# Kernel tuning notes

Hardware: AMD Instinct MI355X
Metric: run time of the kernel (lower is better)

Reference implementation:

```python
import jax, jax.numpy as jnp
import numpy as np
from jax import lax

EPS = 1e-8

def setup_inputs() -> dict:
    key = jax.random.key(0)
    ks = jax.random.split(key, 9)
    B, Cin, H, W = 16, 128, 64, 64
    C = 256
    return {
        "x":  jax.random.normal(ks[0], (B, Cin, H, W), jnp.float32),
        "w1": jax.random.normal(ks[1], (C, Cin, 3, 3), jnp.float32) * 0.02,
        "b1": jax.random.normal(ks[2], (C,), jnp.float32) * 0.02,
        "w2": jax.random.normal(ks[3], (C, C), jnp.float32) * 0.02,
        "b2": jax.random.normal(ks[4], (C,), jnp.float32) * 0.02,
        "w3": jax.random.normal(ks[5], (C, C), jnp.float32) * 0.02,
        "b3": jax.random.normal(ks[6], (C,), jnp.float32) * 0.02,
        "w4": jax.random.normal(ks[7], (C, C), jnp.float32) * 0.02,
        "b4": jax.random.normal(ks[8], (C,), jnp.float32) * 0.02,
    }

def reference(x, w1, b1, w2, b2, w3, b3, w4, b4):
    B = x.shape[0]
    # conv1: 3x3, pad 1 -> [B, 256, H, W]
    conv1 = lax.conv_general_dilated(
        x, w1, window_strides=(1, 1), padding="SAME",
        dimension_numbers=("NCHW", "OIHW", "NCHW")) + b1[None, :, None, None]
    H, W = conv1.shape[2], conv1.shape[3]
    C = conv1.shape[1]
    # gap1 -> [B, 256]; note: forward never applies relu/sigmoid (faithful)
    gap1 = conv1.mean(axis=(2, 3))
    c2 = gap1 @ w2.T + b2            # 1x1 conv on 1x1 spatial == dense
    c3 = c2 @ w3.T + b3              # [B, 256]
    # add1 = conv1 + conv1 * c3 (broadcast scale over spatial)
    add1 = conv1 * (1.0 + c3[:, :, None, None])
    gap2 = add1.mean(axis=(2, 3))    # [B, 256]
    # cosine similarity along channel dim between gap2 and add1 -> [B, H, W]
    num = jnp.einsum("bc,bchw->bhw", gap2, add1)
    n_g = jnp.maximum(jnp.linalg.norm(gap2, axis=1), EPS)[:, None, None]
    n_a = jnp.maximum(jnp.sqrt(jnp.sum(add1 * add1, axis=1)), EPS)
    cos = num / (n_g * n_a)
    r1 = cos.reshape(B, H * W)       # [B, HW]
    m1 = r1.T @ r1                   # [HW, HW] cross-batch position similarity
    # conv4: 1x1 conv -> [B, 256, H, W]
    conv4 = jnp.einsum("oc,bchw->bohw", w4, add1) + b4[None, :, None, None]
    # torch: permute to NHWC then view as [B, 256, HW] (mixes dims; faithful)
    r2 = jnp.transpose(conv4, (0, 2, 3, 1)).reshape(B, C, H * W)
    m2 = r2 @ m1                     # [B, 256, HW]
    return m2.reshape(B, C, H, W)
```

## Files before the change

### kernel.cpp

```cpp
#include <hip/hip_runtime.h>

#define EPSF 1e-8f

typedef __attribute__((ext_vector_type(8))) short bf16x8;
typedef __attribute__((ext_vector_type(16))) float f32x16;

#define MFMA32(a, b, c) __builtin_amdgcn_mfma_f32_32x32x16_bf16(a, b, c, 0, 0, 0)

__device__ __forceinline__ uint32_t splitpack(float v) {
    uint32_t u = __float_as_uint(v);
    uint32_t hb = (u + 0x7fffu + ((u >> 16) & 1u)) & 0xffff0000u;
    float rem = v - __uint_as_float(hb);
    uint32_t r = __float_as_uint(rem);
    uint32_t lb = (r + 0x7fffu + ((r >> 16) & 1u)) >> 16;
    return (hb >> 16) | (lb << 16);
}
__device__ __forceinline__ float unpackf(uint32_t p) {
    return __uint_as_float(p << 16) + __uint_as_float(p & 0xffff0000u);
}

__device__ __forceinline__ void gload_lds16(const void* src, void* dst) {
#if __has_builtin(__builtin_amdgcn_global_load_lds)
    __builtin_amdgcn_global_load_lds(
        (const __attribute__((address_space(1))) uint32_t*)src,
        (__attribute__((address_space(3))) uint32_t*)dst, 16, 0, 0);
#else
    *(uint4*)dst = *(const uint4*)src;
#endif
}

__global__ __launch_bounds__(256) void k_xpack(const float* __restrict__ x,
                                               unsigned short* __restrict__ xph,
                                               unsigned short* __restrict__ xpl) {
    const int bx = blockIdx.x;
    const int hb = bx & 15, cg = (bx >> 4) & 15, b = bx >> 8;
    const int tid = threadIdx.x;
    const int w = tid & 63, hs = tid >> 6;
    const int h = hb * 4 + hs;
    uint32_t hiw[4], low[4];
#pragma unroll
    for (int q = 0; q < 4; ++q) {
        uint32_t u0 = splitpack(x[(((b * 128 + cg * 8 + q * 2) * 64) + h) * 64 + w]);
        uint32_t u1 = splitpack(x[(((b * 128 + cg * 8 + q * 2 + 1) * 64) + h) * 64 + w]);
        hiw[q] = (u0 & 0xffffu) | (u1 << 16);
        low[q] = (u0 >> 16) | (u1 & 0xffff0000u);
    }
    const long o = ((((long)(b * 16 + cg) * 64 + h) * 64) + w) * 8;
    *(uint4*)(xph + o) = *(uint4*)hiw;
    *(uint4*)(xpl + o) = *(uint4*)low;
}

__global__ __launch_bounds__(256) void k_wpack(const float* __restrict__ w1,
                                               short* __restrict__ Bh, short* __restrict__ Bl) {
    int d = blockIdx.x * 256 + threadIdx.x;
    int j = d & 7, lane = (d >> 3) & 63, nt = (d >> 9) & 7, cp = (d >> 12) & 7, tap = d >> 15;
    int oc = nt * 32 + (lane & 31);
    int cin = cp * 16 + (lane >> 5) * 8 + j;
    uint32_t u = splitpack(w1[oc * 1152 + cin * 9 + tap]);
    Bh[d] = (short)(u & 0xffffu);
    Bl[d] = (short)(u >> 16);
}

__global__ __launch_bounds__(512, 4) void k_conv1(
        const unsigned short* __restrict__ xph, const unsigned short* __restrict__ xpl,
        const short* __restrict__ Bh, const short* __restrict__ Bl,
        const float* __restrict__ b1,
        uint32_t* __restrict__ c1p, float* __restrict__ gpart) {
    __shared__ uint4 lds[2 * 2 * 12 * 66];
    const int bx = blockIdx.x;
    const int ot = bx & 1, hp = (bx >> 1) & 15, b = bx >> 5;
    const int h0 = hp * 4;
    const int tid = threadIdx.x;
    const int lane = tid & 63, wv = tid >> 6;
    const int mq = wv >> 1, nh = wv & 1;
    const int l31 = lane & 31, hbit = lane >> 5;

    f32x16 acc[2][2];
#pragma unroll
    for (int i = 0; i < 2; ++i)
#pragma unroll
        for (int j = 0; j < 2; ++j)
#pragma unroll
            for (int r = 0; r < 16; ++r) acc[i][j][r] = 0.f;

    auto stage = [&](int buf, int cp) {
#pragma unroll
        for (int i = 0; i < 3; ++i) {
            const int id = wv * 3 + i;
            const int plane = (id >= 12) ? 1 : 0;
            const int u = id - plane * 12;
            const int r6 = u >> 1, kg = u & 1;
            const int grow = h0 - 1 + r6;
            uint4* dst = &lds[((buf * 2 + plane) * 12 + u) * 66 + 1 + lane];
            if ((unsigned)grow < 64u) {
                const unsigned short* pls = plane ? xpl : xph;
                const unsigned short* src =
                    pls + ((((long)(b * 16 + cp * 2 + kg) * 64 + grow) * 64) + lane) * 8;
                gload_lds16(src, dst);
            } else {
                *dst = (uint4){0u, 0u, 0u, 0u};
            }
        }
    };

    stage(0, 0);
    if (tid < 96) {
        const int row = tid >> 1, side = tid & 1;
        lds[row * 66 + (side ? 65 : 0)] = (uint4){0u, 0u, 0u, 0u};
    }
    __syncthreads();

    int buf = 0;
    for (int cp = 0; cp < 8; ++cp) {
        if (cp < 7) stage(buf ^ 1, cp + 1);
        bf16x8 Bhv[2][2], Blv[2][2];
#define LOADB(tap, par) do {                                                      \
            _Pragma("unroll")                                                     \
            for (int nt = 0; nt < 2; ++nt) {                                      \
                const int fi = (((tap) * 8 + cp) * 8 + ot * 4 + nh * 2 + nt) * 512 + lane * 8; \
                Bhv[par][nt] = *(const bf16x8*)(Bh + fi);                         \
                Blv[par][nt] = *(const bf16x8*)(Bl + fi);                         \
            } } while (0)
        LOADB(0, 0);
#pragma unroll
        for (int tap = 0; tap < 9; ++tap) {
            const int cur = tap & 1, nxt = cur ^ 1;
            if (tap < 8) LOADB(tap + 1, nxt);
            const int kh = tap / 3, kw = tap % 3;
            bf16x8 ah[2], al[2];
#pragma unroll
            for (int mt = 0; mt < 2; ++mt) {
                const int rb = ((buf * 2 + 0) * 12 + (mq + kh) * 2 + hbit) * 66
                               + kw + mt * 32 + l31;
                ah[mt] = *(const bf16x8*)&lds[rb];
                al[mt] = *(const bf16x8*)&lds[rb + 12 * 66];
            }
            __builtin_amdgcn_s_setprio(1);
#pragma unroll
            for (int nt = 0; nt < 2; ++nt)
#pragma unroll
                for (int mt = 0; mt < 2; ++mt) {
                    acc[mt][nt] = MFMA32(ah[mt], Bhv[cur][nt], acc[mt][nt]);
                    acc[mt][nt] = MFMA32(ah[mt], Blv[cur][nt], acc[mt][nt]);
                    acc[mt][nt] = MFMA32(al[mt], Bhv[cur][nt], acc[mt][nt]);
                }
            __builtin_amdgcn_s_setprio(0);
        }
#undef LOADB
        __syncthreads();
        buf ^= 1;
    }

    const int hrow = h0 + mq;
#pragma unroll
    for (int nt = 0; nt < 2; ++nt) {
        const int oc = ot * 128 + (nh * 2 + nt) * 32 + l31;
        float g = 0.f;
#pragma unroll
        for (int mt = 0; mt < 2; ++mt)
#pragma unroll
            for (int r = 0; r < 16; ++r) g += acc[mt][nt][r];
        g += __shfl_xor(g, 32);
        if (hbit == 0) gpart[((b * 16 + hp) * 4 + mq) * 256 + oc] = g;
        const float bias = b1[oc];
#pragma unroll
        for (int mt = 0; mt < 2; ++mt) {
#pragma unroll
            for (int r = 0; r < 16; ++r) {
                const int row = (r & 3) + 8 * (r >> 2) + 4 * hbit;
                const int p = hrow * 64 + mt * 32 + row;
                c1p[((long)(b * 4096 + p)) * 256 + oc] = splitpack(acc[mt][nt][r] + bias);
            }
        }
    }
}

__global__ __launch_bounds__(256) void k_mlp(const float* __restrict__ gpart,
                                             const float* __restrict__ b1,
                                             const float* __restrict__ w2, const float* __restrict__ b2,
                                             const float* __restrict__ w3, const float* __restrict__ b3,
                                             float* __restrict__ scale, float* __restrict__ ga,
                                             float* __restrict__ n_g) {
    int b = blockIdx.x, tid = threadIdx.x;
    __shared__ float gs[256], c2s[256], red[4];
    float g = 0.f;
#pragma unroll 8
    for (int i = 0; i < 64; ++i) g += gpart[(b * 64 + i) * 256 + tid];
    gs[tid] = g * (1.f / 4096.f) + b1[tid];
    __syncthreads();
    {
        const float4* wr = (const float4*)(w2 + tid * 256);
        float a = b2[tid];
#pragma unroll 8
        for (int c4 = 0; c4 < 64; c4++) {
            float4 wv = wr[c4];
            a += wv.x * gs[c4*4] + wv.y * gs[c4*4+1] + wv.z * gs[c4*4+2] + wv.w * gs[c4*4+3];
        }
        c2s[tid] = a;
    }
    __syncthreads();
    float a3 = b3[tid];
    {
        const float4* wr = (const float4*)(w3 + tid * 256);
#pragma unroll 8
        for (int c4 = 0; c4 < 64; c4++) {
            float4 wv = wr[c4];
            a3 += wv.x * c2s[c4*4] + wv.y * c2s[c4*4+1] + wv.z * c2s[c4*4+2] + wv.w * c2s[c4*4+3];
        }
    }
    float s1 = 1.f + a3;
    float g2 = gs[tid] * s1;
    scale[b * 256 + tid] = s1;
    ga[b * 256 + tid] = g2 * s1;
    float r = g2 * g2;
    for (int off = 32; off; off >>= 1) r += __shfl_down(r, off);
    if ((tid & 63) == 0) red[tid >> 6] = r;
    __syncthreads();
    if (tid == 0) n_g[b] = fmaxf(sqrtf(red[0] + red[1] + red[2] + red[3]), EPSF);
}

__global__ __launch_bounds__(256) void k_cos(
        const uint32_t* __restrict__ c1p,
        const float* __restrict__ scale, const float* __restrict__ ga,
        const float* __restrict__ n_g, float* __restrict__ r1) {
    const int bx = blockIdx.x;
    const int pt = bx & 63, b = bx >> 6;
    const int tid = threadIdx.x;
    const int lane = tid & 63, wv = tid >> 6;
    const int half = lane >> 5, l31 = lane & 31;
    float ga8[8], sc8[8];
#pragma unroll
    for (int q = 0; q < 8; ++q) {
        ga8[q] = ga[b * 256 + l31 * 8 + q];
        sc8[q] = scale[b * 256 + l31 * 8 + q];
    }
    const float ng = n_g[b];
#pragma unroll
    for (int pp = 0; pp < 8; ++pp) {
        const int p = pt * 64 + wv * 16 + pp * 2 + half;
        const uint32_t* base = c1p + ((long)(b * 4096 + p)) * 256 + l31 * 8;
        uint4 a = *(const uint4*)base;
        uint4 bq = *(const uint4*)(base + 4);
        uint32_t pk[8] = {a.x, a.y, a.z, a.w, bq.x, bq.y, bq.z, bq.w};
        float num = 0.f, den = 0.f;
#pragma unroll
        for (int q = 0; q < 8; ++q) {
            const float v = unpackf(pk[q]);
            num += ga8[q] * v;
            const float t = sc8[q] * v;
            den += t * t;
        }
#pragma unroll
        for (int off = 1; off <= 16; off <<= 1) {
            num += __shfl_xor(num, off);
            den += __shfl_xor(den, off);
        }
        if (l31 == 0) {
            float na = fmaxf(sqrtf(den), EPSF);
            r1[b * 4096 + p] = num / (ng * na);
        }
    }
}

__global__ __launch_bounds__(256) void k_u(const float* __restrict__ r1,
                                           const float* __restrict__ w4,
                                           const float* __restrict__ b4,
                                           float* __restrict__ Uf, float* __restrict__ Dpart) {
    const int g = blockIdx.x;
    const int tid = threadIdx.x;
    __shared__ float rs[256], red[4];
    rs[tid] = r1[(g >> 4) * 4096 + (g & 15) * 256 + tid];
    __syncthreads();
    float a = 0.f;
#pragma unroll 8
    for (int o = 0; o < 256; ++o) a += rs[o] * w4[o * 256 + tid];
    Uf[(g >> 4) * 4096 + (g & 15) * 256 + tid] = a;
    float d = b4[tid] * rs[tid];
    for (int off = 32; off; off >>= 1) d += __shfl_down(d, off);
    if ((tid & 63) == 0) red[tid >> 6] = d;
    __syncthreads();
    if (tid == 0) Dpart[g] = red[0] + red[1] + red[2] + red[3];
}

__global__ __launch_bounds__(256) void k_t2(const uint32_t* __restrict__ c1p,
                                            const float* __restrict__ Uf,
                                            const float* __restrict__ scale,
                                            const float* __restrict__ Dpart,
                                            float* __restrict__ tmat) {
    __shared__ float Ac[16][256];
    __shared__ float Bc[16][260];
    __shared__ float scs[256];
    const int bx = blockIdx.x;
    const int b = bx >> 4, it = bx & 15;
    const int tid = threadIdx.x;
    const int il = tid >> 4, bp = tid & 15;
    scs[tid] = scale[b * 256 + tid];
    float acc = 0.f;
    for (int jc = 0; jc < 16; ++jc) {
        __syncthreads();
#pragma unroll
        for (int q = 0; q < 4; ++q) {
            const int f4i = tid + q * 256;
            const int row = f4i >> 6, col4 = f4i & 63;
            uint4 u = *(const uint4*)(c1p +
                ((long)(b * 4096 + it * 256 + row * 16 + jc)) * 256 + col4 * 4);
            Ac[row][col4 * 4 + 0] = unpackf(u.x) * scs[col4 * 4 + 0];
            Ac[row][col4 * 4 + 1] = unpackf(u.y) * scs[col4 * 4 + 1];
            Ac[row][col4 * 4 + 2] = unpackf(u.z) * scs[col4 * 4 + 2];
            Ac[row][col4 * 4 + 3] = unpackf(u.w) * scs[col4 * 4 + 3];
            *(float4*)&Bc[row][col4 * 4] =
                *(const float4*)(Uf + (long)row * 4096 + jc * 256 + col4 * 4);
        }
        __syncthreads();
#pragma unroll 8
        for (int j = 0; j < 256; j += 4) {
            float4 a4  = *(const float4*)&Ac[il][j];
            float4 b4v = *(const float4*)&Bc[bp][j];
            acc += a4.x * b4v.x + a4.y * b4v.y + a4.z * b4v.z + a4.w * b4v.w;
        }
    }
    float D = 0.f;
#pragma unroll
    for (int pr = 0; pr < 16; ++pr) D += Dpart[bp * 16 + pr];
    tmat[((b * 256) + it * 16 + il) * 16 + bp] = acc + D;
}

__global__ __launch_bounds__(256) void k_m2(const float* __restrict__ tmat,
                                            const float* __restrict__ r1,
                                            float* __restrict__ outb) {
    __shared__ float r1s[16][512];
    __shared__ float ts[256];
    int bx = blockIdx.x;
    int b = bx >> 7, it = (bx >> 3) & 15, pc = bx & 7;
    int tid = threadIdx.x;
    ts[tid] = tmat[(b * 256 + it * 16) * 16 + tid];
#pragma unroll
    for (int k = 0; k < 8; k++) {
        int f4i = tid + k * 256;
        int row = f4i >> 7, col = f4i & 127;
        *(float4*)&r1s[row][col * 4] = *(const float4*)(r1 + ((long)row << 12) + pc * 512 + col * 4);
    }
    __syncthreads();
    for (int il = 0; il < 16; il++) {
        float tv[16];
#pragma unroll
        for (int bp = 0; bp < 16; bp++) tv[bp] = ts[il * 16 + bp];
#pragma unroll
        for (int k = 0; k < 2; k++) {
            int p = k * 256 + tid;
            float s = 0.f;
#pragma unroll
            for (int bp = 0; bp < 16; bp++) s += tv[bp] * r1s[bp][p];
            outb[((long)b << 20) + ((long)(it * 16 + il) << 12) + pc * 512 + p] = s;
        }
    }
}

extern "C" void kernel_launch(void* const* d_in, const int* in_sizes, int n_in,
                              void* d_out, int out_size, void* d_ws, size_t ws_size,
                              hipStream_t stream) {
    const float* x  = (const float*)d_in[0];
    const float* w1 = (const float*)d_in[1];
    const float* b1 = (const float*)d_in[2];
    const float* w2 = (const float*)d_in[3];
    const float* b2 = (const float*)d_in[4];
    const float* w3 = (const float*)d_in[5];
    const float* b3 = (const float*)d_in[6];
    const float* w4 = (const float*)d_in[7];
    const float* b4 = (const float*)d_in[8];
    float* out = (float*)d_out;

    unsigned short* xph = (unsigned short*)d_out;
    unsigned short* xpl = xph + 8388608L;

    char* p = (char*)d_ws;
    uint32_t* c1p = (uint32_t*)p;  p += 16777216L * 4;
    short* Bh  = (short*)p;  p += 294912L * 2;
    short* Bl  = (short*)p;  p += 294912L * 2;
    float* gpart = (float*)p; p += 262144L * 4;
    float* scale = (float*)p; p += 4096L * 4;
    float* ga    = (float*)p; p += 4096L * 4;
    float* n_g   = (float*)p; p += 16L * 4;
    float* r1    = (float*)p; p += 65536L * 4;
    float* tmat  = (float*)p; p += 65536L * 4;
    float* Uf    = (float*)p; p += 65536L * 4;
    float* Dpart = (float*)p; p += 256L * 4;

    k_xpack <<<4096, 256, 0, stream>>>(x, xph, xpl);
    k_wpack <<<1152, 256, 0, stream>>>(w1, Bh, Bl);
    k_conv1 <<<512,  512, 0, stream>>>(xph, xpl, Bh, Bl, b1, c1p, gpart);
    k_mlp   <<<16,   256, 0, stream>>>(gpart, b1, w2, b2, w3, b3, scale, ga, n_g);
    k_cos   <<<1024, 256, 0, stream>>>(c1p, scale, ga, n_g, r1);
    k_u     <<<256,  256, 0, stream>>>(r1, w4, b4, Uf, Dpart);
    k_t2    <<<256,  256, 0, stream>>>(c1p, Uf, scale, Dpart, tmat);
    k_m2    <<<2048, 256, 0, stream>>>(tmat, r1, out);
}
```

Measured before the change: 252.7 us.

## Deepen conv1 operand prefetch pipeline and swizzle block order

The conv1 MFMA loop now prefetches weight fragments two taps ahead using a triple buffer that carries across channel-pair iterations. It also double-buffers the LDS A-fragment reads one tap ahead, so load latency overlaps with MFMA issue. Block indices are remapped so consecutive blocks land on different batch groups, which changes L2/XCD locality. Launch bounds are relaxed to one block per SM to free registers for the extra buffers, at the cost of lower occupancy.

```diff
diff --git a/kernel.cpp b/kernel.cpp
--- a/kernel.cpp
+++ b/kernel.cpp
@@ -61,13 +61,14 @@
     Bl[d] = (short)(u >> 16);
 }
 
-__global__ __launch_bounds__(512, 4) void k_conv1(
+__global__ __launch_bounds__(512, 1) void k_conv1(
         const unsigned short* __restrict__ xph, const unsigned short* __restrict__ xpl,
         const short* __restrict__ Bh, const short* __restrict__ Bl,
         const float* __restrict__ b1,
         uint32_t* __restrict__ c1p, float* __restrict__ gpart) {
     __shared__ uint4 lds[2 * 2 * 12 * 66];
-    const int bx = blockIdx.x;
+    const int bxr = blockIdx.x;
+    const int bx = ((bxr & 7) << 6) | (bxr >> 3);
     const int ot = bx & 1, hp = (bx >> 1) & 15, b = bx >> 5;
     const int h0 = hp * 4;
     const int tid = threadIdx.x;
@@ -110,46 +111,55 @@
     }
     __syncthreads();
 
+    bf16x8 Ahv[2][2], Alv[2][2], Bhv[3][2], Blv[3][2];
+#define LOADA(tap_, par) do {                                                     \
+        const int kh_ = (tap_) / 3, kw_ = (tap_) % 3;                             \
+        _Pragma("unroll")                                                         \
+        for (int mt = 0; mt < 2; ++mt) {                                          \
+            const int rb = ((buf * 2 + 0) * 12 + (mq + kh_) * 2 + hbit) * 66      \
+                           + kw_ + mt * 32 + l31;                                 \
+            Ahv[par][mt] = *(const bf16x8*)&lds[rb];                              \
+            Alv[par][mt] = *(const bf16x8*)&lds[rb + 12 * 66];                    \
+        } } while (0)
+#define LOADB(cp_, tap_, par) do {                                                \
+        _Pragma("unroll")                                                         \
+        for (int nt = 0; nt < 2; ++nt) {                                          \
+            const int fi = (((tap_) * 8 + (cp_)) * 8 + ot * 4 + nh * 2 + nt) * 512 + lane * 8; \
+            Bhv[par][nt] = *(const bf16x8*)(Bh + fi);                             \
+            Blv[par][nt] = *(const bf16x8*)(Bl + fi);                             \
+        } } while (0)
+
+    LOADB(0, 0, 0);
+    LOADB(0, 1, 1);
     int buf = 0;
     for (int cp = 0; cp < 8; ++cp) {
         if (cp < 7) stage(buf ^ 1, cp + 1);
-        bf16x8 Bhv[2][2], Blv[2][2];
-#define LOADB(tap, par) do {                                                      \
-            _Pragma("unroll")                                                     \
-            for (int nt = 0; nt < 2; ++nt) {                                      \
-                const int fi = (((tap) * 8 + cp) * 8 + ot * 4 + nh * 2 + nt) * 512 + lane * 8; \
-                Bhv[par][nt] = *(const bf16x8*)(Bh + fi);                         \
-                Blv[par][nt] = *(const bf16x8*)(Bl + fi);                         \
-            } } while (0)
-        LOADB(0, 0);
+        LOADA(0, 0);
 #pragma unroll
         for (int tap = 0; tap < 9; ++tap) {
-            const int cur = tap & 1, nxt = cur ^ 1;
-            if (tap < 8) LOADB(tap + 1, nxt);
-            const int kh = tap / 3, kw = tap % 3;
-            bf16x8 ah[2], al[2];
-#pragma unroll
-            for (int mt = 0; mt < 2; ++mt) {
-                const int rb = ((buf * 2 + 0) * 12 + (mq + kh) * 2 + hbit) * 66
-                               + kw + mt * 32 + l31;
-                ah[mt] = *(const bf16x8*)&lds[rb];
-                al[mt] = *(const bf16x8*)&lds[rb + 12 * 66];
+            if (tap < 7) {
+                LOADB(cp, tap + 2, (tap + 2) % 3);
+            } else if (cp < 7) {
+                LOADB(cp + 1, tap - 7, (tap + 2) % 3);
             }
+            if (tap < 8) LOADA(tap + 1, (tap + 1) & 1);
+            const int ab = tap & 1, bb = tap % 3;
             __builtin_amdgcn_s_setprio(1);
 #pragma unroll
             for (int nt = 0; nt < 2; ++nt)
 #pragma unroll
                 for (int mt = 0; mt < 2; ++mt) {
-                    acc[mt][nt] = MFMA32(ah[mt], Bhv[cur][nt], acc[mt][nt]);
-                    acc[mt][nt] = MFMA32(ah[mt], Blv[cur][nt], acc[mt][nt]);
-                    acc[mt][nt] = MFMA32(al[mt], Bhv[cur][nt], acc[mt][nt]);
+                    acc[mt][nt] = MFMA32(Ahv[ab][mt], Bhv[bb][nt], acc[mt][nt]);
+                    acc[mt][nt] = MFMA32(Ahv[ab][mt], Blv[bb][nt], acc[mt][nt]);
+                    acc[mt][nt] = MFMA32(Alv[ab][mt], Bhv[bb][nt], acc[mt][nt]);
                 }
             __builtin_amdgcn_s_setprio(0);
         }
-#undef LOADB
         __syncthreads();
         buf ^= 1;
     }
+#undef LOADA
+#undef LOADB
 
     const int hrow = h0 + mq;
 #pragma unroll
```

New measurement: 224.9 us. -11.0%, faster.

## Split k_t2 reduction four ways, swizzle conv1 block order, hoist B-fragment buffers

Applied to the files above, without the earlier changes.

k_t2 now splits its 16-chunk reduction over four K-slices, launching 1024 blocks instead of 256 on a 256-CU-class GPU. It writes four partial tmat arrays, and k_m2 sums them when loading. conv1's block index is remapped so neighbouring blocks cover different batches and h-tiles, which changes L2/MALL locality and spreads work across XCDs. The B-fragment register arrays are also hoisted out of the cp loop. The cost is extra workspace, more partial-sum traffic, and four global reads per element in k_m2.

```diff
diff --git a/kernel.cpp b/kernel.cpp
--- a/kernel.cpp
+++ b/kernel.cpp
@@ -67,7 +67,8 @@
         const float* __restrict__ b1,
         uint32_t* __restrict__ c1p, float* __restrict__ gpart) {
     __shared__ uint4 lds[2 * 2 * 12 * 66];
-    const int bx = blockIdx.x;
+    const int bxr = blockIdx.x;
+    const int bx = ((bxr & 7) << 6) | (bxr >> 3);
     const int ot = bx & 1, hp = (bx >> 1) & 15, b = bx >> 5;
     const int h0 = hp * 4;
     const int tid = threadIdx.x;
@@ -110,22 +111,22 @@
     }
     __syncthreads();
 
+    bf16x8 Bhv[2][2], Blv[2][2];
+#define LOADB(cp_, tap_, par) do {                                                \
+        _Pragma("unroll")                                                         \
+        for (int nt = 0; nt < 2; ++nt) {                                          \
+            const int fi = (((tap_) * 8 + (cp_)) * 8 + ot * 4 + nh * 2 + nt) * 512 + lane * 8; \
+            Bhv[par][nt] = *(const bf16x8*)(Bh + fi);                             \
+            Blv[par][nt] = *(const bf16x8*)(Bl + fi);                             \
+        } } while (0)
+
     int buf = 0;
     for (int cp = 0; cp < 8; ++cp) {
         if (cp < 7) stage(buf ^ 1, cp + 1);
-        bf16x8 Bhv[2][2], Blv[2][2];
-#define LOADB(tap, par) do {                                                      \
-            _Pragma("unroll")                                                     \
-            for (int nt = 0; nt < 2; ++nt) {                                      \
-                const int fi = (((tap) * 8 + cp) * 8 + ot * 4 + nh * 2 + nt) * 512 + lane * 8; \
-                Bhv[par][nt] = *(const bf16x8*)(Bh + fi);                         \
-                Blv[par][nt] = *(const bf16x8*)(Bl + fi);                         \
-            } } while (0)
-        LOADB(0, 0);
+        LOADB(cp, 0, 0);
 #pragma unroll
         for (int tap = 0; tap < 9; ++tap) {
-            const int cur = tap & 1, nxt = cur ^ 1;
-            if (tap < 8) LOADB(tap + 1, nxt);
+            if (tap < 8) LOADB(cp, tap + 1, (tap + 1) & 1);
             const int kh = tap / 3, kw = tap % 3;
             bf16x8 ah[2], al[2];
 #pragma unroll
@@ -135,21 +136,22 @@
                 ah[mt] = *(const bf16x8*)&lds[rb];
                 al[mt] = *(const bf16x8*)&lds[rb + 12 * 66];
             }
+            const int par = tap & 1;
             __builtin_amdgcn_s_setprio(1);
 #pragma unroll
             for (int nt = 0; nt < 2; ++nt)
 #pragma unroll
                 for (int mt = 0; mt < 2; ++mt) {
-                    acc[mt][nt] = MFMA32(ah[mt], Bhv[cur][nt], acc[mt][nt]);
-                    acc[mt][nt] = MFMA32(ah[mt], Blv[cur][nt], acc[mt][nt]);
-                    acc[mt][nt] = MFMA32(al[mt], Bhv[cur][nt], acc[mt][nt]);
+                    acc[mt][nt] = MFMA32(ah[mt], Bhv[par][nt], acc[mt][nt]);
+                    acc[mt][nt] = MFMA32(ah[mt], Blv[par][nt], acc[mt][nt]);
+                    acc[mt][nt] = MFMA32(al[mt], Bhv[par][nt], acc[mt][nt]);
                 }
             __builtin_amdgcn_s_setprio(0);
         }
-#undef LOADB
         __syncthreads();
         buf ^= 1;
     }
+#undef LOADB
 
     const int hrow = h0 + mq;
 #pragma unroll
@@ -286,17 +288,18 @@
                                             const float* __restrict__ Uf,
                                             const float* __restrict__ scale,
                                             const float* __restrict__ Dpart,
-                                            float* __restrict__ tmat) {
+                                            float* __restrict__ tmat4) {
     __shared__ float Ac[16][256];
     __shared__ float Bc[16][260];
     __shared__ float scs[256];
     const int bx = blockIdx.x;
-    const int b = bx >> 4, it = bx & 15;
+    const int kc = bx >> 8;
+    const int b = (bx >> 4) & 15, it = bx & 15;
     const int tid = threadIdx.x;
     const int il = tid >> 4, bp = tid & 15;
     scs[tid] = scale[b * 256 + tid];
     float acc = 0.f;
-    for (int jc = 0; jc < 16; ++jc) {
+    for (int jc = kc * 4; jc < kc * 4 + 4; ++jc) {
         __syncthreads();
 #pragma unroll
         for (int q = 0; q < 4; ++q) {
@@ -319,13 +322,16 @@
             acc += a4.x * b4v.x + a4.y * b4v.y + a4.z * b4v.z + a4.w * b4v.w;
         }
     }
-    float D = 0.f;
-#pragma unroll
-    for (int pr = 0; pr < 16; ++pr) D += Dpart[bp * 16 + pr];
-    tmat[((b * 256) + it * 16 + il) * 16 + bp] = acc + D;
-}
-
-__global__ __launch_bounds__(256) void k_m2(const float* __restrict__ tmat,
+    if (kc == 0) {
+        float D = 0.f;
+#pragma unroll
+        for (int pr = 0; pr < 16; ++pr) D += Dpart[bp * 16 + pr];
+        acc += D;
+    }
+    tmat4[kc * 65536 + ((b * 256) + it * 16 + il) * 16 + bp] = acc;
+}
+
+__global__ __launch_bounds__(256) void k_m2(const float* __restrict__ tmat4,
                                             const float* __restrict__ r1,
                                             float* __restrict__ outb) {
     __shared__ float r1s[16][512];
@@ -333,7 +339,10 @@
     int bx = blockIdx.x;
     int b = bx >> 7, it = (bx >> 3) & 15, pc = bx & 7;
     int tid = threadIdx.x;
-    ts[tid] = tmat[(b * 256 + it * 16) * 16 + tid];
+    {
+        const int idx = (b * 256 + it * 16) * 16 + tid;
+        ts[tid] = tmat4[idx] + tmat4[65536 + idx] + tmat4[131072 + idx] + tmat4[196608 + idx];
+    }
 #pragma unroll
     for (int k = 0; k < 8; k++) {
         int f4i = tid + k * 256;
@@ -382,7 +391,7 @@
     float* ga    = (float*)p; p += 4096L * 4;
     float* n_g   = (float*)p; p += 16L * 4;
     float* r1    = (float*)p; p += 65536L * 4;
-    float* tmat  = (float*)p; p += 65536L * 4;
+    float* tmat4 = (float*)p; p += 262144L * 4;
     float* Uf    = (float*)p; p += 65536L * 4;
     float* Dpart = (float*)p; p += 256L * 4;
 
@@ -392,6 +401,6 @@
     k_mlp   <<<16,   256, 0, stream>>>(gpart, b1, w2, b2, w3, b3, scale, ga, n_g);
     k_cos   <<<1024, 256, 0, stream>>>(c1p, scale, ga, n_g, r1);
     k_u     <<<256,  256, 0, stream>>>(r1, w4, b4, Uf, Dpart);
-    k_t2    <<<256,  256, 0, stream>>>(c1p, Uf, scale, Dpart, tmat);
-    k_m2    <<<2048, 256, 0, stream>>>(tmat, r1, out);
-}
+    k_t2    <<<1024, 256, 0, stream>>>(c1p, Uf, scale, Dpart, tmat4);
+    k_m2    <<<2048, 256, 0, stream>>>(tmat4, r1, out);
+}
```

Result: slower. 279.5 us (+10.6%).
